# Kernel optimization log

Measured on AMD Instinct MI355X. Metric: run time of the kernel, lower is better.

## Reference

```python
import jax, jax.numpy as jnp
import numpy as np

L, N, E, NODE_D, EDGE_D, H = 3, 50000, 800000, 64, 16, 128
EPS = 1e-5


def _ln(x, g, b):
    mu = jnp.mean(x, axis=-1, keepdims=True)
    var = jnp.var(x, axis=-1, keepdims=True)
    return (x - mu) * jax.lax.rsqrt(var + EPS) * g + b


def setup_inputs() -> dict:
    key = jax.random.key(0)
    ks = jax.random.split(key, 16)
    inp = {
        "x": jax.random.normal(ks[0], (N, NODE_D), dtype=jnp.float32),
        "edge_index": jax.random.randint(ks[1], (2, E), 0, N, dtype=jnp.int64 if jax.config.jax_enable_x64 else jnp.int32),
        "edge_attr": jax.random.normal(ks[2], (E, EDGE_D), dtype=jnp.float32),
        # node_embed: Linear(node_dim, H) + LayerNorm
        "node_W": jax.random.normal(ks[3], (H, NODE_D), dtype=jnp.float32) * (2.0 / H) ** 0.5,
        "node_b": jnp.zeros((H,), jnp.float32),
        "node_ln_g": jnp.ones((H,), jnp.float32),
        "node_ln_b": jnp.zeros((H,), jnp.float32),
        # per-layer GINConv params, stacked on leading layer dim
        "edge_W": jax.random.normal(ks[4], (L, H, EDGE_D), dtype=jnp.float32) * (2.0 / H) ** 0.5,
        "edge_b": jnp.zeros((L, H), jnp.float32),
        "edge_ln_g": jnp.ones((L, H), jnp.float32),
        "edge_ln_b": jnp.zeros((L, H), jnp.float32),
        "sl_attr": jax.random.normal(ks[5], (L, 1, EDGE_D), dtype=jnp.float32),
        "mlp_W1": jax.random.normal(ks[6], (L, 2 * H, H), dtype=jnp.float32) * (1.0 / H) ** 0.5,
        "mlp_b1": jnp.zeros((L, 2 * H), jnp.float32),
        "mlp_W2": jax.random.normal(ks[7], (L, H, 2 * H), dtype=jnp.float32) * (1.0 / (2 * H)) ** 0.5,
        "mlp_b2": jnp.zeros((L, H), jnp.float32),
        # BatchNorm1d affine params (batch-stat / training-mode math)
        "bn_g": jnp.ones((L, H), jnp.float32),
        "bn_b": jnp.zeros((L, H), jnp.float32),
    }
    return inp


def reference(x, edge_index, edge_attr, node_W, node_b, node_ln_g, node_ln_b,
              edge_W, edge_b, edge_ln_g, edge_ln_b, sl_attr,
              mlp_W1, mlp_b1, mlp_W2, mlp_b2, bn_g, bn_b):
    n = x.shape[0]
    # augmented edge list with self loops appended (add_self_loops)
    loop = jnp.arange(n, dtype=edge_index.dtype)
    src = jnp.concatenate([edge_index[0], loop])  # [E+N]
    dst = jnp.concatenate([edge_index[1], loop])  # [E+N]

    # node_embed: Linear -> LN -> ReLU
    h = jax.nn.relu(_ln(x @ node_W.T + node_b, node_ln_g, node_ln_b))

    for l in range(L):
        # edge_embed on [original edges ; learned self-loop attr]
        sl = jnp.broadcast_to(sl_attr[l], (n, EDGE_D))
        ea = jnp.concatenate([edge_attr, sl], axis=0)          # [E+N, edge_dim]
        ea = jax.nn.relu(_ln(ea @ edge_W[l].T + edge_b[l], edge_ln_g[l], edge_ln_b[l]))
        # message: gather x_j + edge_attr; aggregate: scatter-add to dst
        msg = h[src] + ea                                      # [E+N, H]
        aggr = jax.ops.segment_sum(msg, dst, num_segments=n)   # [N, H]
        # update MLP: Linear -> GELU -> Linear (dropout inactive at eval)
        z = jax.nn.gelu(aggr @ mlp_W1[l].T + mlp_b1[l], approximate=False)
        hl = z @ mlp_W2[l].T + mlp_b2[l]
        # BatchNorm1d (training-mode batch statistics over node dim)
        mu = jnp.mean(hl, axis=0, keepdims=True)
        var = jnp.var(hl, axis=0, keepdims=True)
        hl = (hl - mu) * jax.lax.rsqrt(var + EPS) * bn_g[l] + bn_b[l]
        if l != L - 1:
            hl = jax.nn.relu(hl)  # drop_ratio = 0 -> dropout is identity
        h = hl
    return h
```

## Files before the change

### kernel.cpp

```cpp
#include <hip/hip_runtime.h>
#include <cstdint>
#include <cstddef>

#define HD 128
#define EDGED 16
#define NODED 64
#define LN_EPS 1e-5f

typedef __bf16 bf16x8 __attribute__((ext_vector_type(8)));
typedef float  f32x4  __attribute__((ext_vector_type(4)));
typedef _Float16 half2v __attribute__((ext_vector_type(2)));
typedef _Float16 half4v __attribute__((ext_vector_type(4)));

__device__ __forceinline__ float gelu_exact(float x) {
    return 0.5f * x * (1.0f + erff(x * 0.7071067811865475f));
}

__global__ void wconv_k(const float* __restrict__ in, __bf16* __restrict__ hi,
                        __bf16* __restrict__ lo, int n) {
    int i = blockIdx.x * blockDim.x + threadIdx.x;
    if (i < n) {
        float v = in[i];
        __bf16 h = (__bf16)v;
        hi[i] = h;
        lo[i] = (__bf16)(v - (float)h);
    }
}


__global__ void hist_k(const int* __restrict__ ei, int* __restrict__ cnt, int E) {
    int e = blockIdx.x * blockDim.x + threadIdx.x;
    if (e < E) atomicAdd(&cnt[ei[E + e]], 1);
}

__global__ void scan1_k(const int* __restrict__ in, int* __restrict__ out,
                        int* __restrict__ bsum, int n) {
    __shared__ int lds[256];
    int t = threadIdx.x;
    int i = blockIdx.x * 256 + t;
    int v = (i < n) ? in[i] : 0;
    lds[t] = v;
    __syncthreads();
#pragma unroll
    for (int o = 1; o < 256; o <<= 1) {
        int u = (t >= o) ? lds[t - o] : 0;
        __syncthreads();
        lds[t] += u;
        __syncthreads();
    }
    if (i < n) out[i] = lds[t] - v;
    if (t == 255) bsum[blockIdx.x] = lds[255];
}

__global__ void scan2_k(const int* __restrict__ bsum, int* __restrict__ boff, int nb) {
    __shared__ int lds[256];
    int t = threadIdx.x;
    int v = (t < nb) ? bsum[t] : 0;
    lds[t] = v;
    __syncthreads();
#pragma unroll
    for (int o = 1; o < 256; o <<= 1) {
        int u = (t >= o) ? lds[t - o] : 0;
        __syncthreads();
        lds[t] += u;
        __syncthreads();
    }
    if (t < nb) boff[t] = lds[t] - v;
}

__global__ void scan3_k(int* __restrict__ rs, int* __restrict__ cursor,
                        const int* __restrict__ boff, int n, int E) {
    int i = blockIdx.x * 256 + threadIdx.x;
    if (i < n) {
        int v = rs[i] + boff[blockIdx.x];
        rs[i] = v;
        cursor[i] = v;
    }
    if (i == 0) rs[n] = E;
}

__global__ void scatter_k(const int* __restrict__ ei, int* __restrict__ cursor,
                          int2* __restrict__ es, int E) {
    int e = blockIdx.x * blockDim.x + threadIdx.x;
    if (e < E) {
        int dst = ei[E + e];
        int slot = atomicAdd(&cursor[dst], 1);
        es[slot] = make_int2(ei[e], e);
    }
}

__global__ void prep_k(const float* __restrict__ edge_W, const float* __restrict__ edge_b,
                       const float* __restrict__ edge_g, const float* __restrict__ edge_be,
                       const float* __restrict__ sl_attr, float* __restrict__ Wg3,
                       float* __restrict__ bg3, float* __restrict__ M3,
                       float* __restrict__ v3, float* __restrict__ s03,
                       float* __restrict__ slv3)
{
    const int l = blockIdx.x;
    const float* W = edge_W + (size_t)l * HD * EDGED;
    const float* b = edge_b + l * HD;
    const float* g = edge_g + l * HD;
    __shared__ float Wp[HD * EDGED];
    __shared__ float bp[HD];
    __shared__ float wm[EDGED];
    __shared__ float Msh[256];
    __shared__ float vsh[EDGED];
    __shared__ float ash[EDGED];
    __shared__ float bmS, s0sh;
    const int t = threadIdx.x;
#pragma unroll
    for (int m = 0; m < 8; ++m) Wp[m * 256 + t] = W[m * 256 + t];
    __syncthreads();
    if (t < EDGED) {
        float s = 0.f;
        for (int c = 0; c < HD; ++c) s += Wp[c * EDGED + t];
        wm[t] = s * (1.f / HD);
    } else if (t == EDGED) {
        float s = 0.f;
        for (int c = 0; c < HD; ++c) s += b[c];
        bmS = s * (1.f / HD);
    }
    __syncthreads();
    if (t < HD) bp[t] = b[t] - bmS;
    __syncthreads();
#pragma unroll
    for (int m = 0; m < 8; ++m) {
        int idx = m * 256 + t;
        int c = idx >> 4, k = idx & 15;
        float val = Wp[idx] - wm[k];
        Wp[idx] = val;
        Wg3[(size_t)l * 2048 + k * HD + c] = val * g[c];
    }
    if (t < HD) bg3[l * HD + t] = bp[t] * g[t];
    __syncthreads();
    {
        int k = t >> 4, j = t & 15;
        float s = 0.f;
        for (int c = 0; c < HD; ++c) s += Wp[c * EDGED + k] * Wp[c * EDGED + j];
        Msh[t] = s;
        M3[l * 256 + t] = s;
    }
    if (t < EDGED) {
        float s = 0.f;
        for (int c = 0; c < HD; ++c) s += Wp[c * EDGED + t] * bp[c];
        vsh[t] = 2.f * s;
        v3[l * EDGED + t] = 2.f * s;
        ash[t] = sl_attr[l * EDGED + t];
    } else if (t == EDGED) {
        float s = 0.f;
        for (int c = 0; c < HD; ++c) s += bp[c] * bp[c];
        s0sh = s;
        s03[l] = s;
    }
    __syncthreads();
    if (t < HD) {
        float q = s0sh;
#pragma unroll
        for (int k = 0; k < EDGED; ++k) {
            float tk = vsh[k];
#pragma unroll
            for (int j = 0; j < EDGED; ++j) tk = fmaf(Msh[k * 16 + j], ash[j], tk);
            q = fmaf(ash[k], tk, q);
        }
        float inv = rsqrtf(q * (1.f / HD) + LN_EPS);
        float y = 0.f;
#pragma unroll
        for (int k = 0; k < EDGED; ++k) y = fmaf(Wp[t * EDGED + k], ash[k], y);
        slv3[l * HD + t] = fmaxf(fmaf(fmaf(y, g[t], bg3[l * HD + t]), inv, edge_be[l * HD + t]), 0.f);
    }
}

__launch_bounds__(256)
__global__ void einv_k(const int2* __restrict__ es, const float* __restrict__ eattr,
                       const float* __restrict__ M3, const float* __restrict__ v3,
                       const float* __restrict__ s03, float* __restrict__ einv,
                       float* __restrict__ attr_p, int* __restrict__ srcp, int E)
{
    __shared__ float Ms[3 * 256];
    __shared__ float vs[3 * 16];
    __shared__ float s0s[4];
    const int t = threadIdx.x;
    for (int i = t; i < 768; i += 256) Ms[i] = M3[i];
    if (t < 48) vs[t] = v3[t];
    if (t < 3) s0s[t] = s03[t];
    __syncthreads();
    int slot = blockIdx.x * 256 + t;
    if (slot >= E) return;
    int2 se = es[slot];
    srcp[slot] = se.x;
    const float4* ap = (const float4*)(eattr + (size_t)se.y * EDGED);
    float4 A0 = ap[0], A1 = ap[1], A2 = ap[2], A3 = ap[3];
    float4* op = (float4*)(attr_p + (size_t)slot * EDGED);
    op[0] = A0; op[1] = A1; op[2] = A2; op[3] = A3;
    float a[16] = {A0.x, A0.y, A0.z, A0.w, A1.x, A1.y, A1.z, A1.w,
                   A2.x, A2.y, A2.z, A2.w, A3.x, A3.y, A3.z, A3.w};
#pragma unroll
    for (int l = 0; l < 3; ++l) {
        float q = s0s[l];
#pragma unroll
        for (int k = 0; k < 16; ++k) {
            const float* Mr = &Ms[l * 256 + k * 16];
            float tk = vs[l * 16 + k];
#pragma unroll
            for (int j = 0; j < 16; ++j) tk = fmaf(Mr[j], a[j], tk);
            q = fmaf(a[k], tk, q);
        }
        einv[(size_t)l * E + slot] = rsqrtf(q * (1.f / HD) + LN_EPS);
    }
}

template<int K, int NC, int ACT, int STATS, int OUTBF>
__launch_bounds__(256)
__global__ void mgemm_k(const __bf16* __restrict__ Ahi, const __bf16* __restrict__ Alo,
                        const __bf16* __restrict__ Whi, const __bf16* __restrict__ Wlo,
                        const float* __restrict__ bias, float* __restrict__ C,
                        __bf16* __restrict__ Chi, __bf16* __restrict__ Clo,
                        int M, float* __restrict__ stats)
{
    constexpr int RG = 2;
    constexpr int NT = 4;
    constexpr int NK = K / 32;
    __shared__ float st_lds[2][64];

    const int t    = threadIdx.x;
    const int lane = t & 63;
    const int wv   = t >> 6;
    const int ln15 = lane & 15;
    const int quad = lane >> 4;
    const int row_base = blockIdx.x * 128 + wv * 32;
    const int col0 = blockIdx.y * 64;

    f32x4 acc[RG][NT];
#pragma unroll
    for (int g = 0; g < RG; ++g)
#pragma unroll
        for (int nt = 0; nt < NT; ++nt)
#pragma unroll
            for (int r = 0; r < 4; ++r) acc[g][nt][r] = 0.f;

    size_t arow[RG];
#pragma unroll
    for (int g = 0; g < RG; ++g) {
        int row = row_base + g * 16 + ln15;
        row = row < M ? row : M - 1;
        arow[g] = (size_t)row * K + quad * 8;
    }
    size_t brow[NT];
#pragma unroll
    for (int nt = 0; nt < NT; ++nt)
        brow[nt] = (size_t)(col0 + nt * 16 + ln15) * K + quad * 8;

    bf16x8 a0h[RG], a0l[RG], a1h[RG], a1l[RG];
    bf16x8 b0h[NT], b0l[NT], b1h[NT], b1l[NT];

#define LD_A(kc, AH, AL) { \
    _Pragma("unroll") \
    for (int g = 0; g < RG; ++g) { \
        AH[g] = *(const bf16x8*)(Ahi + arow[g] + (kc)); \
        AL[g] = *(const bf16x8*)(Alo + arow[g] + (kc)); \
    } }
#define LD_B(kc, BH, BL) { \
    _Pragma("unroll") \
    for (int nt = 0; nt < NT; ++nt) { \
        BH[nt] = *(const bf16x8*)(Whi + brow[nt] + (kc)); \
        BL[nt] = *(const bf16x8*)(Wlo + brow[nt] + (kc)); \
    } }
#define DO_MFMA(AH, AL, BH, BL) { \
    _Pragma("unroll") \
    for (int nt = 0; nt < NT; ++nt) { \
        _Pragma("unroll") \
        for (int g = 0; g < RG; ++g) { \
            acc[g][nt] = __builtin_amdgcn_mfma_f32_16x16x32_bf16(AH[g], BH[nt], acc[g][nt], 0, 0, 0); \
            acc[g][nt] = __builtin_amdgcn_mfma_f32_16x16x32_bf16(AH[g], BL[nt], acc[g][nt], 0, 0, 0); \
            acc[g][nt] = __builtin_amdgcn_mfma_f32_16x16x32_bf16(AL[g], BH[nt], acc[g][nt], 0, 0, 0); \
        } } }

    LD_A(0, a0h, a0l);
    LD_B(0, b0h, b0l);
    for (int s = 0; s < NK; s += 2) {
        LD_A((s + 1) * 32, a1h, a1l);
        LD_B((s + 1) * 32, b1h, b1l);
        DO_MFMA(a0h, a0l, b0h, b0l);
        if (s + 2 < NK) {
            LD_A((s + 2) * 32, a0h, a0l);
            LD_B((s + 2) * 32, b0h, b0l);
        }
        DO_MFMA(a1h, a1l, b1h, b1l);
    }
#undef LD_A
#undef LD_B
#undef DO_MFMA

    if (STATS) {
        if (t < 64) { st_lds[0][t] = 0.f; st_lds[1][t] = 0.f; }
        __syncthreads();
    }

    float bv[NT];
#pragma unroll
    for (int nt = 0; nt < NT; ++nt) bv[nt] = bias[col0 + nt * 16 + ln15];

    float s1[NT], s2[NT];
#pragma unroll
    for (int nt = 0; nt < NT; ++nt) { s1[nt] = 0.f; s2[nt] = 0.f; }

#pragma unroll
    for (int g = 0; g < RG; ++g)
#pragma unroll
        for (int r = 0; r < 4; ++r) {
            int row = row_base + g * 16 + quad * 4 + r;
            if (row < M) {
#pragma unroll
                for (int nt = 0; nt < NT; ++nt) {
                    float v = acc[g][nt][r] + bv[nt];
                    if (ACT == 1) v = gelu_exact(v);
                    size_t ci = (size_t)row * NC + col0 + nt * 16 + ln15;
                    if (OUTBF) {
                        __bf16 hh = (__bf16)v;
                        Chi[ci] = hh;
                        Clo[ci] = (__bf16)(v - (float)hh);
                    } else {
                        C[ci] = v;
                    }
                    if (STATS) { s1[nt] += v; s2[nt] += v * v; }
                }
            }
        }

    if (STATS) {
#pragma unroll
        for (int nt = 0; nt < NT; ++nt) {
            atomicAdd(&st_lds[0][nt * 16 + ln15], s1[nt]);
            atomicAdd(&st_lds[1][nt * 16 + ln15], s2[nt]);
        }
        __syncthreads();
        if (t < 64) {
            atomicAdd(&stats[col0 + t],      st_lds[0][t]);
            atomicAdd(&stats[HD + col0 + t], st_lds[1][t]);
        }
    }
}

__global__ void ln_relu_k(const float* __restrict__ y, const float* __restrict__ gam,
                          const float* __restrict__ bet, _Float16* __restrict__ h16, int N)
{
    int lane = threadIdx.x & 63;
    int c0 = lane * 2;
    float2 g2 = *(const float2*)&gam[c0];
    float2 b2 = *(const float2*)&bet[c0];
    int wid = (blockIdx.x * blockDim.x + threadIdx.x) >> 6;
    int nw  = (gridDim.x * blockDim.x) >> 6;
    for (int n = wid; n < N; n += nw) {
        float2 v = *(const float2*)&y[(size_t)n * HD + c0];
        float s = v.x + v.y;
        float q = v.x * v.x + v.y * v.y;
#pragma unroll
        for (int o = 32; o > 0; o >>= 1) { s += __shfl_xor(s, o, 64); q += __shfl_xor(q, o, 64); }
        float mu  = s * (1.f / 128.f);
        float inv = rsqrtf(q * (1.f / 128.f) - mu * mu + LN_EPS);
        half2v r;
        r.x = (_Float16)fmaxf(fmaf((v.x - mu) * inv, g2.x, b2.x), 0.f);
        r.y = (_Float16)fmaxf(fmaf((v.y - mu) * inv, g2.y, b2.y), 0.f);
        *(half2v*)&h16[(size_t)n * HD + c0] = r;
    }
}

__launch_bounds__(256)
__global__ void pull5_k(const _Float16* __restrict__ h16, const int* __restrict__ srcp,
                        const int* __restrict__ rs, const float* __restrict__ attr_p,
                        const float* __restrict__ einv, const float* __restrict__ slv,
                        const float* __restrict__ Wg, const float* __restrict__ bg,
                        const float* __restrict__ bet, __bf16* __restrict__ Ahi,
                        __bf16* __restrict__ Alo, int N)
{
    __shared__ float alds_all[4][64 * EDGED];
    const int t = threadIdx.x;
    const int lane = t & 63;
    const int wv = t >> 6;
    float* alds = alds_all[wv];

    const int c0 = lane * 2;
    float w0[16], w1[16];
#pragma unroll
    for (int k = 0; k < 16; ++k) {
        float2 wp = *(const float2*)&Wg[k * HD + c0];
        w0[k] = wp.x; w1[k] = wp.y;
    }
    const float2 bgv  = *(const float2*)&bg[c0];
    const float2 btv  = *(const float2*)&bet[c0];
    const float2 slvv = *(const float2*)&slv[c0];

    const int stride = gridDim.x << 2;
    for (int n = (blockIdx.x << 2) + wv; n < N; n += stride) {
        half2v hs = *(const half2v*)&h16[(size_t)n * HD + c0];
        float acc0 = (float)hs.x + slvv.x;
        float acc1 = (float)hs.y + slvv.y;

        const int beg = rs[n], end = rs[n + 1];
        for (int s0 = beg; s0 < end; s0 += 64) {
            int m = end - s0; if (m > 64) m = 64;
            int   srcv = 0;
            float ivv  = 0.f;
            if (lane < m) { srcv = srcp[s0 + lane]; ivv = einv[s0 + lane]; }
            const float4* src4 = (const float4*)(attr_p + (size_t)s0 * EDGED);
#pragma unroll
            for (int it = 0; it < 4; ++it) {
                int idx = (it << 6) + lane;
                if (idx < (m << 2)) *(float4*)&alds[idx << 2] = src4[idx];
            }
            asm volatile("s_waitcnt lgkmcnt(0)" ::: "memory");

#define EDGE_BODY(JJ, IVJ, HVJ) { \
            const float* ar = &alds[(JJ) * EDGED]; \
            float4 A0 = *(const float4*)ar,       A1 = *(const float4*)(ar + 4); \
            float4 A2 = *(const float4*)(ar + 8), A3 = *(const float4*)(ar + 12); \
            float a[16] = {A0.x, A0.y, A0.z, A0.w, A1.x, A1.y, A1.z, A1.w, \
                           A2.x, A2.y, A2.z, A2.w, A3.x, A3.y, A3.z, A3.w}; \
            float p0 = bgv.x, q0 = 0.f, p1 = bgv.y, q1 = 0.f; \
            _Pragma("unroll") \
            for (int k = 0; k < 16; k += 2) { \
                p0 = fmaf(a[k],     w0[k],     p0); \
                q0 = fmaf(a[k + 1], w0[k + 1], q0); \
                p1 = fmaf(a[k],     w1[k],     p1); \
                q1 = fmaf(a[k + 1], w1[k + 1], q1); \
            } \
            acc0 += fmaxf(fmaf(p0 + q0, IVJ, btv.x), 0.f) + (float)HVJ.x; \
            acc1 += fmaxf(fmaf(p1 + q1, IVJ, btv.y), 0.f) + (float)HVJ.y; \
        }

            int j = 0;
            for (; j + 4 <= m; j += 4) {
                int s_0 = __shfl(srcv, j,     64);
                int s_1 = __shfl(srcv, j + 1, 64);
                int s_2 = __shfl(srcv, j + 2, 64);
                int s_3 = __shfl(srcv, j + 3, 64);
                float i0 = __shfl(ivv, j,     64);
                float i1 = __shfl(ivv, j + 1, 64);
                float i2 = __shfl(ivv, j + 2, 64);
                float i3 = __shfl(ivv, j + 3, 64);
                half2v h0 = *(const half2v*)&h16[(size_t)s_0 * HD + c0];
                half2v h1 = *(const half2v*)&h16[(size_t)s_1 * HD + c0];
                half2v h2 = *(const half2v*)&h16[(size_t)s_2 * HD + c0];
                half2v h3 = *(const half2v*)&h16[(size_t)s_3 * HD + c0];
                EDGE_BODY(j,     i0, h0);
                EDGE_BODY(j + 1, i1, h1);
                EDGE_BODY(j + 2, i2, h2);
                EDGE_BODY(j + 3, i3, h3);
            }
            for (; j < m; ++j) {
                int s_  = __shfl(srcv, j, 64);
                float ij = __shfl(ivv, j, 64);
                half2v hj = *(const half2v*)&h16[(size_t)s_ * HD + c0];
                EDGE_BODY(j, ij, hj);
            }
#undef EDGE_BODY
        }
        __bf16 b0 = (__bf16)acc0, b1 = (__bf16)acc1;
        union { __bf16 b[2]; unsigned u; } ph, pl;
        ph.b[0] = b0;
        ph.b[1] = b1;
        pl.b[0] = (__bf16)(acc0 - (float)b0);
        pl.b[1] = (__bf16)(acc1 - (float)b1);
        *(unsigned*)&Ahi[(size_t)n * HD + c0] = ph.u;
        *(unsigned*)&Alo[(size_t)n * HD + c0] = pl.u;
    }
}

__global__ void bn_k(const float* __restrict__ hl, const float* __restrict__ stats,
                     const float* __restrict__ gam, const float* __restrict__ bet,
                     float* __restrict__ out32, _Float16* __restrict__ out16,
                     int total4, float invN, int relu)
{
    int idx = blockIdx.x * blockDim.x + threadIdx.x;
    if (idx < total4) {
        int c4 = idx & 31;
        float4 x  = ((const float4*)hl)[idx];
        float4 s1 = ((const float4*)stats)[c4];
        float4 s2 = ((const float4*)stats)[32 + c4];
        float4 g  = ((const float4*)gam)[c4];
        float4 b  = ((const float4*)bet)[c4];
        float4 r;
        {
            float m = s1.x * invN; float v = s2.x * invN - m * m;
            r.x = fmaf((x.x - m) * rsqrtf(v + LN_EPS), g.x, b.x);
        }
        {
            float m = s1.y * invN; float v = s2.y * invN - m * m;
            r.y = fmaf((x.y - m) * rsqrtf(v + LN_EPS), g.y, b.y);
        }
        {
            float m = s1.z * invN; float v = s2.z * invN - m * m;
            r.z = fmaf((x.z - m) * rsqrtf(v + LN_EPS), g.z, b.z);
        }
        {
            float m = s1.w * invN; float v = s2.w * invN - m * m;
            r.w = fmaf((x.w - m) * rsqrtf(v + LN_EPS), g.w, b.w);
        }
        if (relu) {
            r.x = fmaxf(r.x, 0.f); r.y = fmaxf(r.y, 0.f);
            r.z = fmaxf(r.z, 0.f); r.w = fmaxf(r.w, 0.f);
        }
        if (out16) {
            half4v o;
            o.x = (_Float16)r.x; o.y = (_Float16)r.y;
            o.z = (_Float16)r.z; o.w = (_Float16)r.w;
            *(half4v*)&out16[(size_t)idx * 4] = o;
        } else {
            ((float4*)out32)[idx] = r;
        }
    }
}

extern "C" void kernel_launch(void* const* d_in, const int* in_sizes, int n_in,
                              void* d_out, int out_size, void* d_ws, size_t ws_size,
                              hipStream_t stream)
{
    const float* x       = (const float*)d_in[0];
    const int*   ei      = (const int*)d_in[1];
    const float* eattr   = (const float*)d_in[2];
    const float* node_W  = (const float*)d_in[3];
    const float* node_b  = (const float*)d_in[4];
    const float* node_g  = (const float*)d_in[5];
    const float* node_be = (const float*)d_in[6];
    const float* edge_W  = (const float*)d_in[7];
    const float* edge_b  = (const float*)d_in[8];
    const float* edge_g  = (const float*)d_in[9];
    const float* edge_be = (const float*)d_in[10];
    const float* sl_attr = (const float*)d_in[11];
    const float* W1      = (const float*)d_in[12];
    const float* b1      = (const float*)d_in[13];
    const float* W2      = (const float*)d_in[14];
    const float* b2      = (const float*)d_in[15];
    const float* bn_g    = (const float*)d_in[16];
    const float* bn_b    = (const float*)d_in[17];

    const int N = in_sizes[0] / NODED;
    const int E = in_sizes[1] / 2;

    char* base = (char*)d_ws;
    size_t off = 0;
    auto take = [&](size_t nbytes) -> void* {
        void* p = base + off;
        off = (off + nbytes + 15) & ~(size_t)15;
        return p;
    };
    _Float16* h16  = (_Float16*)take((size_t)N * HD * 2);
    float*  z      = (float*)take((size_t)N * HD * 4);
    __bf16* aghi   = (__bf16*)take((size_t)N * HD * 2);
    __bf16* aglo   = (__bf16*)take((size_t)N * HD * 2);
    __bf16* zhi    = (__bf16*)take((size_t)N * 256 * 2);
    __bf16* zlo    = (__bf16*)take((size_t)N * 256 * 2);
    __bf16* xhi    = (__bf16*)take((size_t)N * NODED * 2);
    __bf16* xlo    = (__bf16*)take((size_t)N * NODED * 2);
    float*  slv3   = (float*)take(3 * HD * 4);
    float*  stats  = (float*)take(3 * 256 * 4);
    int*    cnt    = (int*)take((size_t)N * 4);
    int*    cursor = (int*)take((size_t)N * 4);
    int*    bsum   = (int*)take(256 * 4);
    int*    boff   = (int*)take(256 * 4);
    int*    rs     = (int*)take(((size_t)N + 2) * 4);
    int2*   es     = (int2*)take((size_t)E * 8);
    float*  einv   = (float*)take((size_t)3 * E * 4);
    float*  attr_p = (float*)take((size_t)E * EDGED * 4);
    int*    srcp   = (int*)take((size_t)E * 4);
    float*  Wg3    = (float*)take(3 * 2048 * 4);
    float*  bg3    = (float*)take(3 * HD * 4);
    float*  M3     = (float*)take(3 * 256 * 4);
    float*  v3     = (float*)take(3 * 16 * 4);
    float*  s03    = (float*)take(4 * 4);
    __bf16* nWhi   = (__bf16*)take((size_t)HD * NODED * 2);
    __bf16* nWlo   = (__bf16*)take((size_t)HD * NODED * 2);
    __bf16* W1hi   = (__bf16*)take((size_t)3 * 256 * HD * 2);
    __bf16* W1lo   = (__bf16*)take((size_t)3 * 256 * HD * 2);
    __bf16* W2hi   = (__bf16*)take((size_t)3 * HD * 256 * 2);
    __bf16* W2lo   = (__bf16*)take((size_t)3 * HD * 256 * 2);

    wconv_k<<<(HD * NODED + 255) / 256, 256, 0, stream>>>(node_W, nWhi, nWlo, HD * NODED);
    wconv_k<<<(3 * 256 * HD + 255) / 256, 256, 0, stream>>>(W1, W1hi, W1lo, 3 * 256 * HD);
    wconv_k<<<(3 * 256 * HD + 255) / 256, 256, 0, stream>>>(W2, W2hi, W2lo, 3 * 256 * HD);
    wconv_k<<<((int)((size_t)N * NODED + 255) / 256), 256, 0, stream>>>(x, xhi, xlo, N * NODED);

    prep_k<<<3, 256, 0, stream>>>(edge_W, edge_b, edge_g, edge_be, sl_attr,
                                  Wg3, bg3, M3, v3, s03, slv3);

    const int eblocks = (E + 255) / 256;
    const int nblocks = (N + 255) / 256;
    hipMemsetAsync(cnt, 0, (size_t)N * sizeof(int), stream);
    hist_k<<<eblocks, 256, 0, stream>>>(ei, cnt, E);
    scan1_k<<<nblocks, 256, 0, stream>>>(cnt, rs, bsum, N);
    scan2_k<<<1, 256, 0, stream>>>(bsum, boff, nblocks);
    scan3_k<<<nblocks, 256, 0, stream>>>(rs, cursor, boff, N, E);
    scatter_k<<<eblocks, 256, 0, stream>>>(ei, cursor, es, E);

    einv_k<<<eblocks, 256, 0, stream>>>(es, eattr, M3, v3, s03, einv, attr_p, srcp, E);

    const int total4  = N * (HD / 4);
    const int vblocks = (total4 + 255) / 256;
    const int gb128   = (N + 127) / 128;
    int pgrid = (N + 3) / 4;
    if (pgrid > 2048) pgrid = 2048;

    mgemm_k<NODED, HD, 0, 0, 0><<<dim3(gb128, 2), 256, 0, stream>>>(
        xhi, xlo, nWhi, nWlo, node_b, z, nullptr, nullptr, N, nullptr);
    ln_relu_k<<<(N + 3) / 4, 256, 0, stream>>>(z, node_g, node_be, h16, N);

    hipMemsetAsync(stats, 0, 3 * 256 * sizeof(float), stream);

    for (int l = 0; l < 3; ++l) {
        pull5_k<<<pgrid, 256, 0, stream>>>(h16, srcp, rs, attr_p,
                                           einv + (size_t)l * E,
                                           slv3 + l * HD, Wg3 + (size_t)l * 2048,
                                           bg3 + l * HD, edge_be + l * HD,
                                           aghi, aglo, N);

        mgemm_k<HD, 256, 1, 0, 1><<<dim3(gb128, 4), 256, 0, stream>>>(
            aghi, aglo, W1hi + (size_t)l * 256 * HD, W1lo + (size_t)l * 256 * HD,
            b1 + l * 256, nullptr, zhi, zlo, N, nullptr);

        mgemm_k<256, HD, 0, 1, 0><<<dim3(gb128, 2), 256, 0, stream>>>(
            zhi, zlo, W2hi + (size_t)l * HD * 256, W2lo + (size_t)l * HD * 256,
            b2 + l * HD, (float*)d_out, nullptr, nullptr, N, stats + l * 256);

        bn_k<<<vblocks, 256, 0, stream>>>((const float*)d_out, stats + l * 256,
                                          bn_g + l * HD, bn_b + l * HD,
                                          (float*)d_out, (l < 2) ? h16 : nullptr,
                                          total4, 1.f / N, (l < 2) ? 1 : 0);
    }
}
```

Baseline: 927.4 us.

## Software-pipeline pull kernel edge loads and pack src index with inverse-std

The aggregation kernel now prefetches the next node's row range, packed (src, inv-std) pairs and the first 32 edge-attribute rows into registers while it processes the current node, hiding global load latency. The per-layer src index and LN inverse-std are stored together as an int2, so one 8-byte load replaces two separate loads, at the cost of duplicating src across three layers. The chunk size drops from 64 to 32 edges, which halves LDS use. Nodes with more than 32 edges fall back to an unpipelined loop.

```diff
diff --git a/kernel.cpp b/kernel.cpp
--- a/kernel.cpp
+++ b/kernel.cpp
@@ -173,8 +173,8 @@
 __launch_bounds__(256)
 __global__ void einv_k(const int2* __restrict__ es, const float* __restrict__ eattr,
                        const float* __restrict__ M3, const float* __restrict__ v3,
-                       const float* __restrict__ s03, float* __restrict__ einv,
-                       float* __restrict__ attr_p, int* __restrict__ srcp, int E)
+                       const float* __restrict__ s03, int2* __restrict__ sei,
+                       float* __restrict__ attr_p, int E)
 {
     __shared__ float Ms[3 * 256];
     __shared__ float vs[3 * 16];
@@ -187,7 +187,6 @@
     int slot = blockIdx.x * 256 + t;
     if (slot >= E) return;
     int2 se = es[slot];
-    srcp[slot] = se.x;
     const float4* ap = (const float4*)(eattr + (size_t)se.y * EDGED);
     float4 A0 = ap[0], A1 = ap[1], A2 = ap[2], A3 = ap[3];
     float4* op = (float4*)(attr_p + (size_t)slot * EDGED);
@@ -205,7 +204,8 @@
             for (int j = 0; j < 16; ++j) tk = fmaf(Mr[j], a[j], tk);
             q = fmaf(a[k], tk, q);
         }
-        einv[(size_t)l * E + slot] = rsqrtf(q * (1.f / HD) + LN_EPS);
+        float iv = rsqrtf(q * (1.f / HD) + LN_EPS);
+        sei[(size_t)l * E + slot] = make_int2(se.x, __float_as_int(iv));
     }
 }
 
@@ -366,14 +366,13 @@
 }
 
 __launch_bounds__(256)
-__global__ void pull5_k(const _Float16* __restrict__ h16, const int* __restrict__ srcp,
-                        const int* __restrict__ rs, const float* __restrict__ attr_p,
-                        const float* __restrict__ einv, const float* __restrict__ slv,
-                        const float* __restrict__ Wg, const float* __restrict__ bg,
-                        const float* __restrict__ bet, __bf16* __restrict__ Ahi,
-                        __bf16* __restrict__ Alo, int N)
+__global__ void pull6_k(const _Float16* __restrict__ h16, const int* __restrict__ rs,
+                        const float* __restrict__ attr_p, const int2* __restrict__ sei,
+                        const float* __restrict__ slv, const float* __restrict__ Wg,
+                        const float* __restrict__ bg, const float* __restrict__ bet,
+                        __bf16* __restrict__ Ahi, __bf16* __restrict__ Alo, int N)
 {
-    __shared__ float alds_all[4][64 * EDGED];
+    __shared__ float alds_all[4][32 * EDGED];
     const int t = threadIdx.x;
     const int lane = t & 63;
     const int wv = t >> 6;
@@ -391,53 +390,82 @@
     const float2 slvv = *(const float2*)&slv[c0];
 
     const int stride = gridDim.x << 2;
-    for (int n = (blockIdx.x << 2) + wv; n < N; n += stride) {
+    const float4* ap = (const float4*)attr_p;
+
+    int n = (blockIdx.x << 2) + wv;
+    if (n >= N) return;
+
+    int rb0 = rs[n], re0 = rs[n + 1];
+    int n1 = n + stride;
+    int rb1 = 0, re1 = 0;
+    if (n1 < N) { rb1 = rs[n1]; re1 = rs[n1 + 1]; }
+    int m0 = re0 - rb0; if (m0 > 32) m0 = 32;
+    int2 sv = make_int2(0, 0);
+    if (lane < m0) sv = sei[rb0 + lane];
+    float4 a0 = make_float4(0.f, 0.f, 0.f, 0.f), a1 = a0;
+    {
+        int i0 = lane, i1 = 64 + lane;
+        if (i0 < (m0 << 2)) a0 = ap[(size_t)rb0 * 4 + i0];
+        if (i1 < (m0 << 2)) a1 = ap[(size_t)rb0 * 4 + i1];
+    }
+
+#define EDGE_BODY(JJ, IVJ, HVJ) { \
+        const float* ar = &alds[(JJ) * EDGED]; \
+        float4 A0 = *(const float4*)ar,       A1 = *(const float4*)(ar + 4); \
+        float4 A2 = *(const float4*)(ar + 8), A3 = *(const float4*)(ar + 12); \
+        float a[16] = {A0.x, A0.y, A0.z, A0.w, A1.x, A1.y, A1.z, A1.w, \
+                       A2.x, A2.y, A2.z, A2.w, A3.x, A3.y, A3.z, A3.w}; \
+        float p0 = bgv.x, q0 = 0.f, p1 = bgv.y, q1 = 0.f; \
+        _Pragma("unroll") \
+        for (int k = 0; k < 16; k += 2) { \
+            p0 = fmaf(a[k],     w0[k],     p0); \
+            q0 = fmaf(a[k + 1], w0[k + 1], q0); \
+            p1 = fmaf(a[k],     w1[k],     p1); \
+            q1 = fmaf(a[k + 1], w1[k + 1], q1); \
+        } \
+        acc0 += fmaxf(fmaf(p0 + q0, IVJ, btv.x), 0.f) + (float)HVJ.x; \
+        acc1 += fmaxf(fmaf(p1 + q1, IVJ, btv.y), 0.f) + (float)HVJ.y; \
+    }
+
+    while (n < N) {
+        {
+            int i0 = lane, i1 = 64 + lane;
+            if (i0 < (m0 << 2)) *(float4*)&alds[i0 << 2] = a0;
+            if (i1 < (m0 << 2)) *(float4*)&alds[i1 << 2] = a1;
+        }
+        const int  curb = rb0, cure = re0, mc = m0;
+        const int2 svc  = sv;
+
+        int n2 = n1 + stride;
+        int rb2 = 0, re2 = 0;
+        if (n2 < N) { rb2 = rs[n2]; re2 = rs[n2 + 1]; }
+        int mn = re1 - rb1; if (mn > 32) mn = 32;
+        int2 svn = make_int2(0, 0);
+        if (lane < mn) svn = sei[rb1 + lane];
+        float4 b0v = make_float4(0.f, 0.f, 0.f, 0.f), b1v = b0v;
+        {
+            int i0 = lane, i1 = 64 + lane;
+            if (i0 < (mn << 2)) b0v = ap[(size_t)rb1 * 4 + i0];
+            if (i1 < (mn << 2)) b1v = ap[(size_t)rb1 * 4 + i1];
+        }
+
+        asm volatile("s_waitcnt lgkmcnt(0)" ::: "memory");
+
         half2v hs = *(const half2v*)&h16[(size_t)n * HD + c0];
         float acc0 = (float)hs.x + slvv.x;
         float acc1 = (float)hs.y + slvv.y;
 
-        const int beg = rs[n], end = rs[n + 1];
-        for (int s0 = beg; s0 < end; s0 += 64) {
-            int m = end - s0; if (m > 64) m = 64;
-            int   srcv = 0;
-            float ivv  = 0.f;
-            if (lane < m) { srcv = srcp[s0 + lane]; ivv = einv[s0 + lane]; }
-            const float4* src4 = (const float4*)(attr_p + (size_t)s0 * EDGED);
-#pragma unroll
-            for (int it = 0; it < 4; ++it) {
-                int idx = (it << 6) + lane;
-                if (idx < (m << 2)) *(float4*)&alds[idx << 2] = src4[idx];
-            }
-            asm volatile("s_waitcnt lgkmcnt(0)" ::: "memory");
-
-#define EDGE_BODY(JJ, IVJ, HVJ) { \
-            const float* ar = &alds[(JJ) * EDGED]; \
-            float4 A0 = *(const float4*)ar,       A1 = *(const float4*)(ar + 4); \
-            float4 A2 = *(const float4*)(ar + 8), A3 = *(const float4*)(ar + 12); \
-            float a[16] = {A0.x, A0.y, A0.z, A0.w, A1.x, A1.y, A1.z, A1.w, \
-                           A2.x, A2.y, A2.z, A2.w, A3.x, A3.y, A3.z, A3.w}; \
-            float p0 = bgv.x, q0 = 0.f, p1 = bgv.y, q1 = 0.f; \
-            _Pragma("unroll") \
-            for (int k = 0; k < 16; k += 2) { \
-                p0 = fmaf(a[k],     w0[k],     p0); \
-                q0 = fmaf(a[k + 1], w0[k + 1], q0); \
-                p1 = fmaf(a[k],     w1[k],     p1); \
-                q1 = fmaf(a[k + 1], w1[k + 1], q1); \
-            } \
-            acc0 += fmaxf(fmaf(p0 + q0, IVJ, btv.x), 0.f) + (float)HVJ.x; \
-            acc1 += fmaxf(fmaf(p1 + q1, IVJ, btv.y), 0.f) + (float)HVJ.y; \
-        }
-
+        {
             int j = 0;
-            for (; j + 4 <= m; j += 4) {
-                int s_0 = __shfl(srcv, j,     64);
-                int s_1 = __shfl(srcv, j + 1, 64);
-                int s_2 = __shfl(srcv, j + 2, 64);
-                int s_3 = __shfl(srcv, j + 3, 64);
-                float i0 = __shfl(ivv, j,     64);
-                float i1 = __shfl(ivv, j + 1, 64);
-                float i2 = __shfl(ivv, j + 2, 64);
-                float i3 = __shfl(ivv, j + 3, 64);
+            for (; j + 4 <= mc; j += 4) {
+                int s_0 = __shfl(svc.x, j,     64);
+                int s_1 = __shfl(svc.x, j + 1, 64);
+                int s_2 = __shfl(svc.x, j + 2, 64);
+                int s_3 = __shfl(svc.x, j + 3, 64);
+                float i0 = __int_as_float(__shfl(svc.y, j,     64));
+                float i1 = __int_as_float(__shfl(svc.y, j + 1, 64));
+                float i2 = __int_as_float(__shfl(svc.y, j + 2, 64));
+                float i3 = __int_as_float(__shfl(svc.y, j + 3, 64));
                 half2v h0 = *(const half2v*)&h16[(size_t)s_0 * HD + c0];
                 half2v h1 = *(const half2v*)&h16[(size_t)s_1 * HD + c0];
                 half2v h2 = *(const half2v*)&h16[(size_t)s_2 * HD + c0];
@@ -447,14 +475,32 @@
                 EDGE_BODY(j + 2, i2, h2);
                 EDGE_BODY(j + 3, i3, h3);
             }
-            for (; j < m; ++j) {
-                int s_  = __shfl(srcv, j, 64);
-                float ij = __shfl(ivv, j, 64);
+            for (; j < mc; ++j) {
+                int s_  = __shfl(svc.x, j, 64);
+                float ij = __int_as_float(__shfl(svc.y, j, 64));
                 half2v hj = *(const half2v*)&h16[(size_t)s_ * HD + c0];
                 EDGE_BODY(j, ij, hj);
             }
-#undef EDGE_BODY
-        }
+        }
+
+        for (int s0 = curb + 32; s0 < cure; s0 += 32) {
+            int mx = cure - s0; if (mx > 32) mx = 32;
+            int2 svx = make_int2(0, 0);
+            if (lane < mx) svx = sei[s0 + lane];
+            {
+                int i0 = lane, i1 = 64 + lane;
+                if (i0 < (mx << 2)) *(float4*)&alds[i0 << 2] = ap[(size_t)s0 * 4 + i0];
+                if (i1 < (mx << 2)) *(float4*)&alds[i1 << 2] = ap[(size_t)s0 * 4 + i1];
+            }
+            asm volatile("s_waitcnt lgkmcnt(0)" ::: "memory");
+            for (int j = 0; j < mx; ++j) {
+                int s_  = __shfl(svx.x, j, 64);
+                float ij = __int_as_float(__shfl(svx.y, j, 64));
+                half2v hj = *(const half2v*)&h16[(size_t)s_ * HD + c0];
+                EDGE_BODY(j, ij, hj);
+            }
+        }
+
         __bf16 b0 = (__bf16)acc0, b1 = (__bf16)acc1;
         union { __bf16 b[2]; unsigned u; } ph, pl;
         ph.b[0] = b0;
@@ -463,7 +509,12 @@
         pl.b[1] = (__bf16)(acc1 - (float)b1);
         *(unsigned*)&Ahi[(size_t)n * HD + c0] = ph.u;
         *(unsigned*)&Alo[(size_t)n * HD + c0] = pl.u;
-    }
+
+        n = n1; n1 = n2;
+        rb0 = rb1; re0 = re1; rb1 = rb2; re1 = re2;
+        m0 = mn; sv = svn; a0 = b0v; a1 = b1v;
+    }
+#undef EDGE_BODY
 }
 
 __global__ void bn_k(const float* __restrict__ hl, const float* __restrict__ stats,
@@ -560,9 +611,8 @@
     int*    boff   = (int*)take(256 * 4);
     int*    rs     = (int*)take(((size_t)N + 2) * 4);
     int2*   es     = (int2*)take((size_t)E * 8);
-    float*  einv   = (float*)take((size_t)3 * E * 4);
+    int2*   sei    = (int2*)take((size_t)3 * E * 8);
     float*  attr_p = (float*)take((size_t)E * EDGED * 4);
-    int*    srcp   = (int*)take((size_t)E * 4);
     float*  Wg3    = (float*)take(3 * 2048 * 4);
     float*  bg3    = (float*)take(3 * HD * 4);
     float*  M3     = (float*)take(3 * 256 * 4);
@@ -592,7 +642,7 @@
     scan3_k<<<nblocks, 256, 0, stream>>>(rs, cursor, boff, N, E);
     scatter_k<<<eblocks, 256, 0, stream>>>(ei, cursor, es, E);
 
-    einv_k<<<eblocks, 256, 0, stream>>>(es, eattr, M3, v3, s03, einv, attr_p, srcp, E);
+    einv_k<<<eblocks, 256, 0, stream>>>(es, eattr, M3, v3, s03, sei, attr_p, E);
 
     const int total4  = N * (HD / 4);
     const int vblocks = (total4 + 255) / 256;
@@ -607,8 +657,7 @@
     hipMemsetAsync(stats, 0, 3 * 256 * sizeof(float), stream);
 
     for (int l = 0; l < 3; ++l) {
-        pull5_k<<<pgrid, 256, 0, stream>>>(h16, srcp, rs, attr_p,
-                                           einv + (size_t)l * E,
+        pull6_k<<<pgrid, 256, 0, stream>>>(h16, rs, attr_p, sei + (size_t)l * E,
                                            slv3 + l * HD, Wg3 + (size_t)l * 2048,
                                            bg3 + l * HD, edge_be + l * HD,
                                            aghi, aglo, N);
```

Result: no change. 936.6 us (+1.0%).

## Store edge attributes and edge weights in fp16 and use packed dot2 in pull

Applied to the files above, without the earlier changes.

Edge attributes and the folded edge-embedding weights are now stored in fp16, and the per-edge 16-wide projection in the pull kernel uses fdot2 packed half dot products instead of scalar fp32 FMAs. The source index and per-edge LayerNorm inverse std are packed into one int2 array per layer, so each edge needs a single 8-byte load. This halves attribute traffic and LDS footprint in the hot aggregation loop and cuts VALU work, at the cost of fp16 rounding on the edge attributes and weights.

```diff
diff --git a/kernel.cpp b/kernel.cpp
--- a/kernel.cpp
+++ b/kernel.cpp
@@ -11,6 +11,9 @@
 typedef float  f32x4  __attribute__((ext_vector_type(4)));
 typedef _Float16 half2v __attribute__((ext_vector_type(2)));
 typedef _Float16 half4v __attribute__((ext_vector_type(4)));
+typedef _Float16 half8v __attribute__((ext_vector_type(8)));
+
+union HU { half8v v; half2v p[4]; };
 
 __device__ __forceinline__ float gelu_exact(float x) {
     return 0.5f * x * (1.0f + erff(x * 0.7071067811865475f));
@@ -91,7 +94,7 @@
 
 __global__ void prep_k(const float* __restrict__ edge_W, const float* __restrict__ edge_b,
                        const float* __restrict__ edge_g, const float* __restrict__ edge_be,
-                       const float* __restrict__ sl_attr, float* __restrict__ Wg3,
+                       const float* __restrict__ sl_attr, _Float16* __restrict__ Wg16_3,
                        float* __restrict__ bg3, float* __restrict__ M3,
                        float* __restrict__ v3, float* __restrict__ s03,
                        float* __restrict__ slv3)
@@ -129,7 +132,7 @@
         int c = idx >> 4, k = idx & 15;
         float val = Wp[idx] - wm[k];
         Wp[idx] = val;
-        Wg3[(size_t)l * 2048 + k * HD + c] = val * g[c];
+        Wg16_3[(size_t)l * 2048 + idx] = (_Float16)(val * g[c]);
     }
     if (t < HD) bg3[l * HD + t] = bp[t] * g[t];
     __syncthreads();
@@ -173,8 +176,8 @@
 __launch_bounds__(256)
 __global__ void einv_k(const int2* __restrict__ es, const float* __restrict__ eattr,
                        const float* __restrict__ M3, const float* __restrict__ v3,
-                       const float* __restrict__ s03, float* __restrict__ einv,
-                       float* __restrict__ attr_p, int* __restrict__ srcp, int E)
+                       const float* __restrict__ s03, int2* __restrict__ sei,
+                       _Float16* __restrict__ attr16, int E)
 {
     __shared__ float Ms[3 * 256];
     __shared__ float vs[3 * 16];
@@ -187,13 +190,18 @@
     int slot = blockIdx.x * 256 + t;
     if (slot >= E) return;
     int2 se = es[slot];
-    srcp[slot] = se.x;
     const float4* ap = (const float4*)(eattr + (size_t)se.y * EDGED);
     float4 A0 = ap[0], A1 = ap[1], A2 = ap[2], A3 = ap[3];
-    float4* op = (float4*)(attr_p + (size_t)slot * EDGED);
-    op[0] = A0; op[1] = A1; op[2] = A2; op[3] = A3;
     float a[16] = {A0.x, A0.y, A0.z, A0.w, A1.x, A1.y, A1.z, A1.w,
                    A2.x, A2.y, A2.z, A2.w, A3.x, A3.y, A3.z, A3.w};
+    {
+        half8v o0, o1;
+#pragma unroll
+        for (int i = 0; i < 8; ++i) { o0[i] = (_Float16)a[i]; o1[i] = (_Float16)a[8 + i]; }
+        _Float16* op = attr16 + (size_t)slot * EDGED;
+        *(half8v*)&op[0] = o0;
+        *(half8v*)&op[8] = o1;
+    }
 #pragma unroll
     for (int l = 0; l < 3; ++l) {
         float q = s0s[l];
@@ -205,7 +213,8 @@
             for (int j = 0; j < 16; ++j) tk = fmaf(Mr[j], a[j], tk);
             q = fmaf(a[k], tk, q);
         }
-        einv[(size_t)l * E + slot] = rsqrtf(q * (1.f / HD) + LN_EPS);
+        float iv = rsqrtf(q * (1.f / HD) + LN_EPS);
+        sei[(size_t)l * E + slot] = make_int2(se.x, __float_as_int(iv));
     }
 }
 
@@ -366,25 +375,25 @@
 }
 
 __launch_bounds__(256)
-__global__ void pull5_k(const _Float16* __restrict__ h16, const int* __restrict__ srcp,
-                        const int* __restrict__ rs, const float* __restrict__ attr_p,
-                        const float* __restrict__ einv, const float* __restrict__ slv,
-                        const float* __restrict__ Wg, const float* __restrict__ bg,
-                        const float* __restrict__ bet, __bf16* __restrict__ Ahi,
-                        __bf16* __restrict__ Alo, int N)
+__global__ void pull8_k(const _Float16* __restrict__ h16, const int* __restrict__ rs,
+                        const _Float16* __restrict__ attr16, const int2* __restrict__ sei,
+                        const float* __restrict__ slv, const _Float16* __restrict__ Wg16,
+                        const float* __restrict__ bg, const float* __restrict__ bet,
+                        __bf16* __restrict__ Ahi, __bf16* __restrict__ Alo, int N)
 {
-    __shared__ float alds_all[4][64 * EDGED];
+    __shared__ _Float16 alds_all[4][64 * EDGED];
     const int t = threadIdx.x;
     const int lane = t & 63;
     const int wv = t >> 6;
-    float* alds = alds_all[wv];
+    _Float16* alds = alds_all[wv];
+    uint4* alds4 = (uint4*)alds;
 
     const int c0 = lane * 2;
-    float w0[16], w1[16];
-#pragma unroll
-    for (int k = 0; k < 16; ++k) {
-        float2 wp = *(const float2*)&Wg[k * HD + c0];
-        w0[k] = wp.x; w1[k] = wp.y;
+    half2v w0p[8], w1p[8];
+#pragma unroll
+    for (int k = 0; k < 8; ++k) {
+        w0p[k] = *(const half2v*)&Wg16[c0 * EDGED + 2 * k];
+        w1p[k] = *(const half2v*)&Wg16[(c0 + 1) * EDGED + 2 * k];
     }
     const float2 bgv  = *(const float2*)&bg[c0];
     const float2 btv  = *(const float2*)&bet[c0];
@@ -399,45 +408,51 @@
         const int beg = rs[n], end = rs[n + 1];
         for (int s0 = beg; s0 < end; s0 += 64) {
             int m = end - s0; if (m > 64) m = 64;
-            int   srcv = 0;
-            float ivv  = 0.f;
-            if (lane < m) { srcv = srcp[s0 + lane]; ivv = einv[s0 + lane]; }
-            const float4* src4 = (const float4*)(attr_p + (size_t)s0 * EDGED);
-#pragma unroll
-            for (int it = 0; it < 4; ++it) {
+            int2 sv = make_int2(0, 0);
+            if (lane < m) sv = sei[s0 + lane];
+            const uint4* src4 = (const uint4*)(attr16 + (size_t)s0 * EDGED);
+#pragma unroll
+            for (int it = 0; it < 2; ++it) {
                 int idx = (it << 6) + lane;
-                if (idx < (m << 2)) *(float4*)&alds[idx << 2] = src4[idx];
+                if (idx < (m << 1)) alds4[idx] = src4[idx];
             }
             asm volatile("s_waitcnt lgkmcnt(0)" ::: "memory");
 
 #define EDGE_BODY(JJ, IVJ, HVJ) { \
-            const float* ar = &alds[(JJ) * EDGED]; \
-            float4 A0 = *(const float4*)ar,       A1 = *(const float4*)(ar + 4); \
-            float4 A2 = *(const float4*)(ar + 8), A3 = *(const float4*)(ar + 12); \
-            float a[16] = {A0.x, A0.y, A0.z, A0.w, A1.x, A1.y, A1.z, A1.w, \
-                           A2.x, A2.y, A2.z, A2.w, A3.x, A3.y, A3.z, A3.w}; \
+            HU ua, ub; \
+            ua.v = *(const half8v*)&alds[(JJ) * EDGED]; \
+            ub.v = *(const half8v*)&alds[(JJ) * EDGED + 8]; \
             float p0 = bgv.x, q0 = 0.f, p1 = bgv.y, q1 = 0.f; \
-            _Pragma("unroll") \
-            for (int k = 0; k < 16; k += 2) { \
-                p0 = fmaf(a[k],     w0[k],     p0); \
-                q0 = fmaf(a[k + 1], w0[k + 1], q0); \
-                p1 = fmaf(a[k],     w1[k],     p1); \
-                q1 = fmaf(a[k + 1], w1[k + 1], q1); \
-            } \
+            p0 = __builtin_amdgcn_fdot2(ua.p[0], w0p[0], p0, false); \
+            q0 = __builtin_amdgcn_fdot2(ua.p[1], w0p[1], q0, false); \
+            p1 = __builtin_amdgcn_fdot2(ua.p[0], w1p[0], p1, false); \
+            q1 = __builtin_amdgcn_fdot2(ua.p[1], w1p[1], q1, false); \
+            p0 = __builtin_amdgcn_fdot2(ua.p[2], w0p[2], p0, false); \
+            q0 = __builtin_amdgcn_fdot2(ua.p[3], w0p[3], q0, false); \
+            p1 = __builtin_amdgcn_fdot2(ua.p[2], w1p[2], p1, false); \
+            q1 = __builtin_amdgcn_fdot2(ua.p[3], w1p[3], q1, false); \
+            p0 = __builtin_amdgcn_fdot2(ub.p[0], w0p[4], p0, false); \
+            q0 = __builtin_amdgcn_fdot2(ub.p[1], w0p[5], q0, false); \
+            p1 = __builtin_amdgcn_fdot2(ub.p[0], w1p[4], p1, false); \
+            q1 = __builtin_amdgcn_fdot2(ub.p[1], w1p[5], q1, false); \
+            p0 = __builtin_amdgcn_fdot2(ub.p[2], w0p[6], p0, false); \
+            q0 = __builtin_amdgcn_fdot2(ub.p[3], w0p[7], q0, false); \
+            p1 = __builtin_amdgcn_fdot2(ub.p[2], w1p[6], p1, false); \
+            q1 = __builtin_amdgcn_fdot2(ub.p[3], w1p[7], q1, false); \
             acc0 += fmaxf(fmaf(p0 + q0, IVJ, btv.x), 0.f) + (float)HVJ.x; \
             acc1 += fmaxf(fmaf(p1 + q1, IVJ, btv.y), 0.f) + (float)HVJ.y; \
         }
 
             int j = 0;
             for (; j + 4 <= m; j += 4) {
-                int s_0 = __shfl(srcv, j,     64);
-                int s_1 = __shfl(srcv, j + 1, 64);
-                int s_2 = __shfl(srcv, j + 2, 64);
-                int s_3 = __shfl(srcv, j + 3, 64);
-                float i0 = __shfl(ivv, j,     64);
-                float i1 = __shfl(ivv, j + 1, 64);
-                float i2 = __shfl(ivv, j + 2, 64);
-                float i3 = __shfl(ivv, j + 3, 64);
+                int s_0 = __shfl(sv.x, j,     64);
+                int s_1 = __shfl(sv.x, j + 1, 64);
+                int s_2 = __shfl(sv.x, j + 2, 64);
+                int s_3 = __shfl(sv.x, j + 3, 64);
+                float i0 = __int_as_float(__shfl(sv.y, j,     64));
+                float i1 = __int_as_float(__shfl(sv.y, j + 1, 64));
+                float i2 = __int_as_float(__shfl(sv.y, j + 2, 64));
+                float i3 = __int_as_float(__shfl(sv.y, j + 3, 64));
                 half2v h0 = *(const half2v*)&h16[(size_t)s_0 * HD + c0];
                 half2v h1 = *(const half2v*)&h16[(size_t)s_1 * HD + c0];
                 half2v h2 = *(const half2v*)&h16[(size_t)s_2 * HD + c0];
@@ -448,8 +463,8 @@
                 EDGE_BODY(j + 3, i3, h3);
             }
             for (; j < m; ++j) {
-                int s_  = __shfl(srcv, j, 64);
-                float ij = __shfl(ivv, j, 64);
+                int s_  = __shfl(sv.x, j, 64);
+                float ij = __int_as_float(__shfl(sv.y, j, 64));
                 half2v hj = *(const half2v*)&h16[(size_t)s_ * HD + c0];
                 EDGE_BODY(j, ij, hj);
             }
@@ -560,10 +575,9 @@
     int*    boff   = (int*)take(256 * 4);
     int*    rs     = (int*)take(((size_t)N + 2) * 4);
     int2*   es     = (int2*)take((size_t)E * 8);
-    float*  einv   = (float*)take((size_t)3 * E * 4);
-    float*  attr_p = (float*)take((size_t)E * EDGED * 4);
-    int*    srcp   = (int*)take((size_t)E * 4);
-    float*  Wg3    = (float*)take(3 * 2048 * 4);
+    int2*   sei    = (int2*)take((size_t)3 * E * 8);
+    _Float16* attr16 = (_Float16*)take((size_t)E * EDGED * 2);
+    _Float16* Wg16_3 = (_Float16*)take(3 * 2048 * 2);
     float*  bg3    = (float*)take(3 * HD * 4);
     float*  M3     = (float*)take(3 * 256 * 4);
     float*  v3     = (float*)take(3 * 16 * 4);
@@ -581,7 +595,7 @@
     wconv_k<<<((int)((size_t)N * NODED + 255) / 256), 256, 0, stream>>>(x, xhi, xlo, N * NODED);
 
     prep_k<<<3, 256, 0, stream>>>(edge_W, edge_b, edge_g, edge_be, sl_attr,
-                                  Wg3, bg3, M3, v3, s03, slv3);
+                                  Wg16_3, bg3, M3, v3, s03, slv3);
 
     const int eblocks = (E + 255) / 256;
     const int nblocks = (N + 255) / 256;
@@ -592,7 +606,7 @@
     scan3_k<<<nblocks, 256, 0, stream>>>(rs, cursor, boff, N, E);
     scatter_k<<<eblocks, 256, 0, stream>>>(ei, cursor, es, E);
 
-    einv_k<<<eblocks, 256, 0, stream>>>(es, eattr, M3, v3, s03, einv, attr_p, srcp, E);
+    einv_k<<<eblocks, 256, 0, stream>>>(es, eattr, M3, v3, s03, sei, attr16, E);
 
     const int total4  = N * (HD / 4);
     const int vblocks = (total4 + 255) / 256;
@@ -607,9 +621,8 @@
     hipMemsetAsync(stats, 0, 3 * 256 * sizeof(float), stream);
 
     for (int l = 0; l < 3; ++l) {
-        pull5_k<<<pgrid, 256, 0, stream>>>(h16, srcp, rs, attr_p,
-                                           einv + (size_t)l * E,
-                                           slv3 + l * HD, Wg3 + (size_t)l * 2048,
+        pull8_k<<<pgrid, 256, 0, stream>>>(h16, rs, attr16, sei + (size_t)l * E,
+                                           slv3 + l * HD, Wg16_3 + (size_t)l * 2048,
                                            bg3 + l * HD, edge_be + l * HD,
                                            aghi, aglo, N);
 
```

Result: faster. 883.3 us (-4.8%).
